# Kernel tuning notes

Hardware: AMD Instinct MI355X
Metric: run time of the kernel (lower is better)

## Reference

```python
import jax, jax.numpy as jnp
import numpy as np

B, N, C, D, H, O = 32, 2048, 16, 128, 128, 128


def setup_inputs():
    key = jax.random.key(0)
    ks = jax.random.split(key, 6)
    childrenList = jax.random.randint(ks[0], (B, N, C), 0, N)
    nodeEmb = jax.random.normal(ks[1], (B, N, D), dtype=jnp.float32)
    std1 = 1.0 / np.sqrt(D)
    W1 = jax.random.normal(ks[2], (3 * D, H), dtype=jnp.float32) * std1
    b1 = jax.random.normal(ks[3], (H,), dtype=jnp.float32) * (2.0 * std1)
    std2 = 1.0 / np.sqrt(H)
    W2 = jax.random.normal(ks[4], (H, O), dtype=jnp.float32) * std2
    b2 = jax.random.normal(ks[5], (O,), dtype=jnp.float32) * (2.0 * std2)
    return {"childrenList": childrenList, "nodeEmb": nodeEmb,
            "W1": W1, "b1": b1, "W2": W2, "b2": b2}


def _gather_feature(children, emb):
    # children: [B,N,C] int (0 = padding/no child), emb: [B,N,D]
    Bx, Nx, Dx = emb.shape
    # index 0 must look up a zero vector (padding child)
    lookup = jnp.concatenate([jnp.zeros((Bx, 1, Dx), emb.dtype), emb[:, 1:, :]], axis=1)
    child_emb = jax.vmap(lambda lu, ch: lu[ch])(lookup, children)      # [B,N,C,D]
    return jnp.concatenate([emb[:, :, None, :], child_emb], axis=2)    # [B,N,C+1,D]


def _conv_weights(children):
    # TBCNN positional coefficients eta_t / eta_r / eta_l (Mou et al.)
    Bx, Nx, Cx = children.shape
    f32 = jnp.float32
    mask = (children > 0).astype(f32)                                   # [B,N,C]
    t = jnp.concatenate([jnp.ones((Bx, Nx, 1), f32),
                         jnp.zeros((Bx, Nx, Cx), f32)], axis=2)        # parent=1, children=0
    num_sib = jnp.sum(mask, axis=2, keepdims=True)                      # [B,N,1]
    pos = jnp.arange(1, Cx + 1, dtype=f32)                              # 1-based child position
    r_child = jnp.where(num_sib == 1, 0.5 * mask,
                        mask * (pos - 1.0) / jnp.maximum(num_sib - 1.0, 1.0))
    r = jnp.concatenate([jnp.zeros((Bx, Nx, 1), f32), r_child], axis=2)
    full_mask = jnp.concatenate([jnp.ones((Bx, Nx, 1), f32), mask], axis=2)
    l = (1.0 - t) * (1.0 - r) * full_mask
    return jnp.stack([t, r, l], axis=-1)                                # [B,N,C+1,3]


def reference(childrenList, nodeEmb, W1, b1, W2, b2):
    feature = _gather_feature(childrenList, nodeEmb)                    # [B,N,C+1,D]
    weights = _conv_weights(childrenList)                               # [B,N,C+1,3]
    wf = jnp.einsum('bnck,bncd->bnkd', weights, feature)                # [B,N,3,D]
    wf = wf.reshape(wf.shape[0], wf.shape[1], -1)                       # [B,N,3D]
    h = jnp.tanh(wf @ W1 + b1)                                          # [B,N,H]
    pooled = jnp.max(h, axis=1)                                         # [B,H] max-pool over nodes
    out = jnp.tanh(pooled @ W2 + b2)                                    # [B,O]
    half = out.shape[0] // 2
    v1, v2 = out[:half], out[half:]
    eps = 1e-8
    n1 = jnp.maximum(jnp.linalg.norm(v1, axis=1), eps)
    n2 = jnp.maximum(jnp.linalg.norm(v2, axis=1), eps)
    return jnp.sum(v1 * v2, axis=1) / (n1 * n2)                         # [B/2]
```

## Files before the change

### kernel.cpp

```cpp
#include <hip/hip_runtime.h>

#define NB 32
#define NN 2048
#define NC 16
#define ND 128
#define NH 128
#define NK 384
#define TM 32
#define NBLK (NB * (NN / TM))

typedef __bf16 bf16x8 __attribute__((ext_vector_type(8)));
typedef float f32x4 __attribute__((ext_vector_type(4)));

__device__ __forceinline__ unsigned short f2bf(float f){
  unsigned u = __float_as_uint(f);
  u = (u + 0x7fffu + ((u >> 16) & 1u)) >> 16;
  return (unsigned short)u;
}
__device__ __forceinline__ unsigned enc_f32(float x){
  unsigned u = __float_as_uint(x);
  return (u & 0x80000000u) ? ~u : (u | 0x80000000u);
}
__device__ __forceinline__ float dec_f32(unsigned u){
  return __uint_as_float((u & 0x80000000u) ? (u & 0x7fffffffu) : ~u);
}

__device__ __forceinline__ void stq(unsigned char* base, int stride, int row, int koff, uint4 u){
  *(uint4*)(base + row * stride + (koff ^ ((row & 7) << 4))) = u;
}
__device__ __forceinline__ void st8(unsigned char* base, int stride, int row, int koff, const float* f){
  uint4 u;
  u.x = (unsigned)f2bf(f[0]) | ((unsigned)f2bf(f[1]) << 16);
  u.y = (unsigned)f2bf(f[2]) | ((unsigned)f2bf(f[3]) << 16);
  u.z = (unsigned)f2bf(f[4]) | ((unsigned)f2bf(f[5]) << 16);
  u.w = (unsigned)f2bf(f[6]) | ((unsigned)f2bf(f[7]) << 16);
  stq(base, stride, row, koff, u);
}
__device__ __forceinline__ uint4 ldq(const unsigned char* base, int stride, int row, int koff){
  return *(const uint4*)(base + row * stride + (koff ^ ((row & 7) << 4)));
}

#define OFF_POOLED 0
#define OFF_W1     16384
#define OFF_W2     114688
#define OFF_EMB    147456
#define WS_NEED_BF (147456 + (size_t)NB*NN*ND*2)

__global__ __launch_bounds__(256) void tbcnn_prep(
    const float* __restrict__ nodeEmb, const float* __restrict__ W1,
    const float* __restrict__ W2, unsigned* __restrict__ pooled,
    uint4* __restrict__ w1frag, uint4* __restrict__ w2frag,
    ushort* __restrict__ embBf, int doEmb)
{
  const int blk = blockIdx.x;
  const int t = threadIdx.x;
  if (blk < 2048){
    if (!doEmb) return;
    const float4* src = (const float4*)nodeEmb;
    const int tid = blk * 256 + t;
    #pragma unroll
    for (int it = 0; it < 4; ++it){
      const int i = tid + it * 524288;
      float4 v = src[i];
      ushort4 o;
      o.x = f2bf(v.x); o.y = f2bf(v.y); o.z = f2bf(v.z); o.w = f2bf(v.w);
      *(ushort4*)(embBf + (size_t)i * 4) = o;
    }
  } else if (blk < 2072){
    const int tt = (blk - 2048) * 256 + t;
    if (tt < NB * NH) pooled[tt] = 0u;
    const int lane = tt & 63;
    const int rest = tt >> 6;
    const int ks = rest % 12;
    const int cf = rest / 12;
    const int col = (cf >> 1) * 32 + (cf & 1) * 16 + (lane & 15);
    const int k0 = ks * 32 + (lane >> 4) * 8;
    unsigned ps[4];
    #pragma unroll
    for (int p = 0; p < 4; ++p){
      unsigned lo = f2bf(W1[(size_t)(k0 + 2*p) * NH + col]);
      unsigned hi = f2bf(W1[(size_t)(k0 + 2*p + 1) * NH + col]);
      ps[p] = lo | (hi << 16);
    }
    w1frag[tt] = make_uint4(ps[0], ps[1], ps[2], ps[3]);
  } else {
    const int tt = (blk - 2072) * 256 + t;
    const int lane = tt & 63;
    const int rest = tt >> 6;
    const int ks = rest & 3;
    const int cf = rest >> 2;
    const int col = (cf >> 1) * 32 + (cf & 1) * 16 + (lane & 15);
    const int k0 = ks * 32 + (lane >> 4) * 8;
    unsigned ps[4];
    #pragma unroll
    for (int p = 0; p < 4; ++p){
      unsigned lo = f2bf(W2[(size_t)(k0 + 2*p) * NH + col]);
      unsigned hi = f2bf(W2[(size_t)(k0 + 2*p + 1) * NH + col]);
      ps[p] = lo | (hi << 16);
    }
    w2frag[tt] = make_uint4(ps[0], ps[1], ps[2], ps[3]);
  }
}

#define PROCU(u, i) { \
  float lo_ = __uint_as_float((u) << 16); \
  float hi_ = __uint_as_float((u) & 0xffff0000u); \
  aR[(i)]   += wrc * lo_; aL[(i)]   += wlc * lo_; \
  aR[(i)+1] += wrc * hi_; aL[(i)+1] += wlc * hi_; }

template<bool BF>
__global__ __launch_bounds__(256, 2) void tbcnn_main(
    const int* __restrict__ children, const float* __restrict__ nodeEmb,
    const ushort* __restrict__ embBf, const uint4* __restrict__ w1frag,
    unsigned* __restrict__ pooled)
{
  __shared__ __align__(16) unsigned char wf_raw[TM * 768];
  const int j0 = ((blockIdx.x & 7) << 8) | (blockIdx.x >> 3);
  const int b    = j0 >> 6;
  const int tile = j0 & 63;
  const int n0 = tile * TM;
  const int t = threadIdx.x;
  const int lane = t & 63;
  const int w = t >> 6;

  {
    const int nloc = t >> 3;
    const int q = t & 7;
    const int d0 = q * 16;
    const int gn = n0 + nloc;
    const int4* chp4 = (const int4*)(children + ((size_t)b * NN + gn) * NC);

    int ns = 0;
    #pragma unroll
    for (int c4 = 0; c4 < 4; ++c4){
      int4 v = chp4[c4];
      ns += (v.x > 0) + (v.y > 0) + (v.z > 0) + (v.w > 0);
    }
    const float rdiv = 1.0f / (float)(((ns - 1) > 1) ? (ns - 1) : 1);
    const bool one_sib = (ns == 1);

    if (BF){
      const ushort* sp = embBf + ((size_t)b * NN + gn) * ND + d0;
      stq(wf_raw, 768, nloc, 2 * d0,       *(const uint4*)sp);
      stq(wf_raw, 768, nloc, 2 * (d0 + 8), *(const uint4*)(sp + 8));
    } else {
      const float* sp = nodeEmb + ((size_t)b * NN + gn) * ND + d0;
      float sv[16];
      #pragma unroll
      for (int j = 0; j < 4; ++j){
        float4 s = *(const float4*)(sp + j * 4);
        sv[j*4+0]=s.x; sv[j*4+1]=s.y; sv[j*4+2]=s.z; sv[j*4+3]=s.w;
      }
      st8(wf_raw, 768, nloc, 2 * d0, sv);
      st8(wf_raw, 768, nloc, 2 * (d0 + 8), sv + 8);
    }

    float aR[16], aL[16];
    #pragma unroll
    for (int i = 0; i < 16; ++i){ aR[i] = 0.0f; aL[i] = 0.0f; }
    #pragma unroll
    for (int c4 = 0; c4 < 4; ++c4){
      int4 v = chp4[c4];
      int cidx[4] = {v.x, v.y, v.z, v.w};
      #pragma unroll
      for (int jj = 0; jj < 4; ++jj){
        const int c = c4 * 4 + jj;
        const int idx = cidx[jj];
        const float mk  = (idx > 0) ? 1.0f : 0.0f;
        const float wrc = one_sib ? (0.5f * mk) : (mk * (float)c * rdiv);
        const float wlc = (1.0f - wrc) * mk;
        if (BF){
          const ushort* cp = embBf + ((size_t)b * NN + idx) * ND + d0;
          uint4 u0 = *(const uint4*)cp;
          uint4 u1 = *(const uint4*)(cp + 8);
          PROCU(u0.x, 0)  PROCU(u0.y, 2)  PROCU(u0.z, 4)  PROCU(u0.w, 6)
          PROCU(u1.x, 8)  PROCU(u1.y, 10) PROCU(u1.z, 12) PROCU(u1.w, 14)
        } else {
          const float* cp = nodeEmb + ((size_t)b * NN + idx) * ND + d0;
          #pragma unroll
          for (int j = 0; j < 4; ++j){
            float4 u = *(const float4*)(cp + j * 4);
            aR[j*4+0] += wrc * u.x; aL[j*4+0] += wlc * u.x;
            aR[j*4+1] += wrc * u.y; aL[j*4+1] += wlc * u.y;
            aR[j*4+2] += wrc * u.z; aL[j*4+2] += wlc * u.z;
            aR[j*4+3] += wrc * u.w; aL[j*4+3] += wlc * u.w;
          }
        }
      }
    }
    st8(wf_raw, 768, nloc, 2 * (ND + d0),         aR);
    st8(wf_raw, 768, nloc, 2 * (ND + d0 + 8),     aR + 8);
    st8(wf_raw, 768, nloc, 2 * (2 * ND + d0),     aL);
    st8(wf_raw, 768, nloc, 2 * (2 * ND + d0 + 8), aL + 8);
  }
  __syncthreads();

  f32x4 acc[2][2];
  #pragma unroll
  for (int rf = 0; rf < 2; ++rf){
    acc[rf][0] = (f32x4){0.f, 0.f, 0.f, 0.f};
    acc[rf][1] = (f32x4){0.f, 0.f, 0.f, 0.f};
  }
  #pragma unroll 4
  for (int ks = 0; ks < 12; ++ks){
    bf16x8 B0 = __builtin_bit_cast(bf16x8, w1frag[((w * 2 + 0) * 12 + ks) * 64 + lane]);
    bf16x8 B1 = __builtin_bit_cast(bf16x8, w1frag[((w * 2 + 1) * 12 + ks) * 64 + lane]);
    const int koff = ks * 64 + ((lane >> 4) << 4);
    #pragma unroll
    for (int rf = 0; rf < 2; ++rf){
      const int row = rf * 16 + (lane & 15);
      bf16x8 a = __builtin_bit_cast(bf16x8, ldq(wf_raw, 768, row, koff));
      acc[rf][0] = __builtin_amdgcn_mfma_f32_16x16x32_bf16(a, B0, acc[rf][0], 0, 0, 0);
      acc[rf][1] = __builtin_amdgcn_mfma_f32_16x16x32_bf16(a, B1, acc[rf][1], 0, 0, 0);
    }
  }

  float m0 = -3.0e38f, m1 = -3.0e38f;
  #pragma unroll
  for (int rf = 0; rf < 2; ++rf)
    #pragma unroll
    for (int i = 0; i < 4; ++i){
      m0 = fmaxf(m0, acc[rf][0][i]);
      m1 = fmaxf(m1, acc[rf][1][i]);
    }
  m0 = fmaxf(m0, __shfl_xor(m0, 16, 64));
  m0 = fmaxf(m0, __shfl_xor(m0, 32, 64));
  m1 = fmaxf(m1, __shfl_xor(m1, 16, 64));
  m1 = fmaxf(m1, __shfl_xor(m1, 32, 64));
  if (lane < 16){
    atomicMax(pooled + b * NH + w * 32 + lane,      enc_f32(m0));
    atomicMax(pooled + b * NH + w * 32 + 16 + lane, enc_f32(m1));
  }
}

__global__ __launch_bounds__(256) void tbcnn_final(
    const unsigned* __restrict__ pooled, const float* __restrict__ b1,
    const uint4* __restrict__ w2frag, const float* __restrict__ b2,
    float* __restrict__ out)
{
  __shared__ __align__(16) unsigned char hls[NB * 256];
  __shared__ float os[NB * NH];
  const int t = threadIdx.x;
  const int lane = t & 63;
  const int w = t >> 6;

  {
    const int row = t >> 3;
    const int q = t & 7;
    const int d0 = q * 16;
    const unsigned* pp = pooled + row * NH + d0;
    const float* bp = b1 + d0;
    float hv[16];
    #pragma unroll
    for (int j = 0; j < 16; ++j) hv[j] = tanhf(dec_f32(pp[j]) + bp[j]);
    st8(hls, 256, row, 2 * d0, hv);
    st8(hls, 256, row, 2 * (d0 + 8), hv + 8);
  }
  __syncthreads();

  f32x4 acc[2][2];
  #pragma unroll
  for (int rf = 0; rf < 2; ++rf){
    acc[rf][0] = (f32x4){0.f, 0.f, 0.f, 0.f};
    acc[rf][1] = (f32x4){0.f, 0.f, 0.f, 0.f};
  }
  #pragma unroll
  for (int ks = 0; ks < 4; ++ks){
    bf16x8 B0 = __builtin_bit_cast(bf16x8, w2frag[((w * 2 + 0) * 4 + ks) * 64 + lane]);
    bf16x8 B1 = __builtin_bit_cast(bf16x8, w2frag[((w * 2 + 1) * 4 + ks) * 64 + lane]);
    const int koff = ks * 64 + ((lane >> 4) << 4);
    #pragma unroll
    for (int rf = 0; rf < 2; ++rf){
      const int row = rf * 16 + (lane & 15);
      bf16x8 a = __builtin_bit_cast(bf16x8, ldq(hls, 256, row, koff));
      acc[rf][0] = __builtin_amdgcn_mfma_f32_16x16x32_bf16(a, B0, acc[rf][0], 0, 0, 0);
      acc[rf][1] = __builtin_amdgcn_mfma_f32_16x16x32_bf16(a, B1, acc[rf][1], 0, 0, 0);
    }
  }

  #pragma unroll
  for (int rf = 0; rf < 2; ++rf)
    #pragma unroll
    for (int cf = 0; cf < 2; ++cf){
      const int col = w * 32 + cf * 16 + (lane & 15);
      const float bias = b2[col];
      #pragma unroll
      for (int i = 0; i < 4; ++i){
        const int r = rf * 16 + (lane >> 4) * 4 + i;
        os[r * NH + col] = tanhf(acc[rf][cf][i] + bias);
      }
    }
  __syncthreads();

  if (t < 16){
    float s12 = 0.f, s11 = 0.f, s22 = 0.f;
    #pragma unroll 4
    for (int d = 0; d < NH; ++d){
      float a = os[t * NH + d];
      float c = os[(t + 16) * NH + d];
      s12 += a * c; s11 += a * a; s22 += c * c;
    }
    float n1 = fmaxf(sqrtf(s11), 1e-8f);
    float n2 = fmaxf(sqrtf(s22), 1e-8f);
    out[t] = s12 / (n1 * n2);
  }
}

extern "C" void kernel_launch(void* const* d_in, const int* in_sizes, int n_in,
                              void* d_out, int out_size, void* d_ws, size_t ws_size,
                              hipStream_t stream)
{
  const int*   children = (const int*)d_in[0];
  const float* nodeEmb  = (const float*)d_in[1];
  const float* W1       = (const float*)d_in[2];
  const float* b1       = (const float*)d_in[3];
  const float* W2       = (const float*)d_in[4];
  const float* b2       = (const float*)d_in[5];
  float* out = (float*)d_out;

  unsigned* pooled = (unsigned*)((char*)d_ws + OFF_POOLED);
  uint4* w1frag    = (uint4*)((char*)d_ws + OFF_W1);
  uint4* w2frag    = (uint4*)((char*)d_ws + OFF_W2);
  ushort* embBf    = (ushort*)((char*)d_ws + OFF_EMB);

  const bool bf = (ws_size >= WS_NEED_BF);

  tbcnn_prep<<<2080, 256, 0, stream>>>(nodeEmb, W1, W2, pooled, w1frag, w2frag, embBf, bf ? 1 : 0);
  if (bf)
    tbcnn_main<true><<<NBLK, 256, 0, stream>>>(children, nodeEmb, embBf, w1frag, pooled);
  else
    tbcnn_main<false><<<NBLK, 256, 0, stream>>>(children, nodeEmb, embBf, w1frag, pooled);
  tbcnn_final<<<1, 256, 0, stream>>>(pooled, b1, w2frag, b2, out);
}
```

Before: 49.45 us.

## Fuse final MLP into main kernel via last-block counter, widen blocks to 512 threads

Removes the separate final kernel launch: each main block increments a global done counter and the last block computes the W2 layer, tanh and cosine similarity, reading pooled values via atomics. The main kernel now uses 512 threads per 32-node tile, so each thread gathers 8 features instead of 16 and each wave computes one 16-column MFMA slice. The prep kernel's embedding conversion is remapped so the chunks it writes follow the main kernel's block order. The cost is an extra atomic and two barriers per block, plus a serial tail in the last block; the wider blocks trade register pressure for more threads sharing each tile.

```diff
diff --git a/kernel.cpp b/kernel.cpp
--- a/kernel.cpp
+++ b/kernel.cpp
@@ -43,24 +43,25 @@
 #define OFF_POOLED 0
 #define OFF_W1     16384
 #define OFF_W2     114688
-#define OFF_EMB    147456
-#define WS_NEED_BF (147456 + (size_t)NB*NN*ND*2)
+#define OFF_DONE   147456
+#define OFF_EMB    147712
+#define WS_NEED_BF (OFF_EMB + (size_t)NB*NN*ND*2)
 
 __global__ __launch_bounds__(256) void tbcnn_prep(
     const float* __restrict__ nodeEmb, const float* __restrict__ W1,
     const float* __restrict__ W2, unsigned* __restrict__ pooled,
     uint4* __restrict__ w1frag, uint4* __restrict__ w2frag,
-    ushort* __restrict__ embBf, int doEmb)
+    ushort* __restrict__ embBf, unsigned* __restrict__ done, int doEmb)
 {
   const int blk = blockIdx.x;
   const int t = threadIdx.x;
   if (blk < 2048){
     if (!doEmb) return;
+    const int chk = ((blk & 7) << 8) | (blk >> 3);
     const float4* src = (const float4*)nodeEmb;
-    const int tid = blk * 256 + t;
     #pragma unroll
     for (int it = 0; it < 4; ++it){
-      const int i = tid + it * 524288;
+      const int i = chk * 1024 + it * 256 + t;
       float4 v = src[i];
       ushort4 o;
       o.x = f2bf(v.x); o.y = f2bf(v.y); o.z = f2bf(v.z); o.w = f2bf(v.w);
@@ -69,6 +70,7 @@
   } else if (blk < 2072){
     const int tt = (blk - 2048) * 256 + t;
     if (tt < NB * NH) pooled[tt] = 0u;
+    if (tt == NB * NH) *done = 0u;
     const int lane = tt & 63;
     const int rest = tt >> 6;
     const int ks = rest % 12;
@@ -109,24 +111,26 @@
   aR[(i)+1] += wrc * hi_; aL[(i)+1] += wlc * hi_; }
 
 template<bool BF>
-__global__ __launch_bounds__(256, 2) void tbcnn_main(
+__global__ __launch_bounds__(512, 8) void tbcnn_main(
     const int* __restrict__ children, const float* __restrict__ nodeEmb,
     const ushort* __restrict__ embBf, const uint4* __restrict__ w1frag,
-    unsigned* __restrict__ pooled)
+    const uint4* __restrict__ w2frag, const float* __restrict__ b1,
+    const float* __restrict__ b2, unsigned* __restrict__ pooled,
+    unsigned* __restrict__ done, float* __restrict__ out)
 {
   __shared__ __align__(16) unsigned char wf_raw[TM * 768];
+  __shared__ unsigned last_flag;
   const int j0 = ((blockIdx.x & 7) << 8) | (blockIdx.x >> 3);
   const int b    = j0 >> 6;
-  const int tile = j0 & 63;
-  const int n0 = tile * TM;
+  const int n0 = (j0 & 63) * TM;
   const int t = threadIdx.x;
   const int lane = t & 63;
   const int w = t >> 6;
 
   {
-    const int nloc = t >> 3;
-    const int q = t & 7;
-    const int d0 = q * 16;
+    const int nloc = t >> 4;
+    const int q = t & 15;
+    const int d0 = q * 8;
     const int gn = n0 + nloc;
     const int4* chp4 = (const int4*)(children + ((size_t)b * NN + gn) * NC);
 
@@ -138,26 +142,24 @@
     }
     const float rdiv = 1.0f / (float)(((ns - 1) > 1) ? (ns - 1) : 1);
     const bool one_sib = (ns == 1);
+    const size_t rowbase = (size_t)b * NN;
 
     if (BF){
-      const ushort* sp = embBf + ((size_t)b * NN + gn) * ND + d0;
-      stq(wf_raw, 768, nloc, 2 * d0,       *(const uint4*)sp);
-      stq(wf_raw, 768, nloc, 2 * (d0 + 8), *(const uint4*)(sp + 8));
+      const ushort* sp = embBf + (rowbase + gn) * ND + d0;
+      stq(wf_raw, 768, nloc, 2 * d0, *(const uint4*)sp);
     } else {
-      const float* sp = nodeEmb + ((size_t)b * NN + gn) * ND + d0;
-      float sv[16];
-      #pragma unroll
-      for (int j = 0; j < 4; ++j){
-        float4 s = *(const float4*)(sp + j * 4);
-        sv[j*4+0]=s.x; sv[j*4+1]=s.y; sv[j*4+2]=s.z; sv[j*4+3]=s.w;
-      }
+      const float* sp = nodeEmb + (rowbase + gn) * ND + d0;
+      float sv[8];
+      float4 s0 = *(const float4*)sp;
+      float4 s1 = *(const float4*)(sp + 4);
+      sv[0]=s0.x; sv[1]=s0.y; sv[2]=s0.z; sv[3]=s0.w;
+      sv[4]=s1.x; sv[5]=s1.y; sv[6]=s1.z; sv[7]=s1.w;
       st8(wf_raw, 768, nloc, 2 * d0, sv);
-      st8(wf_raw, 768, nloc, 2 * (d0 + 8), sv + 8);
-    }
-
-    float aR[16], aL[16];
-    #pragma unroll
-    for (int i = 0; i < 16; ++i){ aR[i] = 0.0f; aL[i] = 0.0f; }
+    }
+
+    float aR[8], aL[8];
+    #pragma unroll
+    for (int i = 0; i < 8; ++i){ aR[i] = 0.0f; aL[i] = 0.0f; }
     #pragma unroll
     for (int c4 = 0; c4 < 4; ++c4){
       int4 v = chp4[c4];
@@ -170,128 +172,110 @@
         const float wrc = one_sib ? (0.5f * mk) : (mk * (float)c * rdiv);
         const float wlc = (1.0f - wrc) * mk;
         if (BF){
-          const ushort* cp = embBf + ((size_t)b * NN + idx) * ND + d0;
-          uint4 u0 = *(const uint4*)cp;
-          uint4 u1 = *(const uint4*)(cp + 8);
-          PROCU(u0.x, 0)  PROCU(u0.y, 2)  PROCU(u0.z, 4)  PROCU(u0.w, 6)
-          PROCU(u1.x, 8)  PROCU(u1.y, 10) PROCU(u1.z, 12) PROCU(u1.w, 14)
+          uint4 u = *(const uint4*)(embBf + (rowbase + idx) * ND + d0);
+          PROCU(u.x, 0) PROCU(u.y, 2) PROCU(u.z, 4) PROCU(u.w, 6)
         } else {
-          const float* cp = nodeEmb + ((size_t)b * NN + idx) * ND + d0;
-          #pragma unroll
-          for (int j = 0; j < 4; ++j){
-            float4 u = *(const float4*)(cp + j * 4);
-            aR[j*4+0] += wrc * u.x; aL[j*4+0] += wlc * u.x;
-            aR[j*4+1] += wrc * u.y; aL[j*4+1] += wlc * u.y;
-            aR[j*4+2] += wrc * u.z; aL[j*4+2] += wlc * u.z;
-            aR[j*4+3] += wrc * u.w; aL[j*4+3] += wlc * u.w;
-          }
+          const float* cp = nodeEmb + (rowbase + idx) * ND + d0;
+          float4 u0 = *(const float4*)cp;
+          float4 u1 = *(const float4*)(cp + 4);
+          aR[0] += wrc * u0.x; aL[0] += wlc * u0.x;
+          aR[1] += wrc * u0.y; aL[1] += wlc * u0.y;
+          aR[2] += wrc * u0.z; aL[2] += wlc * u0.z;
+          aR[3] += wrc * u0.w; aL[3] += wlc * u0.w;
+          aR[4] += wrc * u1.x; aL[4] += wlc * u1.x;
+          aR[5] += wrc * u1.y; aL[5] += wlc * u1.y;
+          aR[6] += wrc * u1.z; aL[6] += wlc * u1.z;
+          aR[7] += wrc * u1.w; aL[7] += wlc * u1.w;
         }
       }
     }
-    st8(wf_raw, 768, nloc, 2 * (ND + d0),         aR);
-    st8(wf_raw, 768, nloc, 2 * (ND + d0 + 8),     aR + 8);
-    st8(wf_raw, 768, nloc, 2 * (2 * ND + d0),     aL);
-    st8(wf_raw, 768, nloc, 2 * (2 * ND + d0 + 8), aL + 8);
-  }
-  __syncthreads();
-
-  f32x4 acc[2][2];
-  #pragma unroll
-  for (int rf = 0; rf < 2; ++rf){
-    acc[rf][0] = (f32x4){0.f, 0.f, 0.f, 0.f};
-    acc[rf][1] = (f32x4){0.f, 0.f, 0.f, 0.f};
-  }
-  #pragma unroll 4
-  for (int ks = 0; ks < 12; ++ks){
-    bf16x8 B0 = __builtin_bit_cast(bf16x8, w1frag[((w * 2 + 0) * 12 + ks) * 64 + lane]);
-    bf16x8 B1 = __builtin_bit_cast(bf16x8, w1frag[((w * 2 + 1) * 12 + ks) * 64 + lane]);
-    const int koff = ks * 64 + ((lane >> 4) << 4);
-    #pragma unroll
-    for (int rf = 0; rf < 2; ++rf){
-      const int row = rf * 16 + (lane & 15);
-      bf16x8 a = __builtin_bit_cast(bf16x8, ldq(wf_raw, 768, row, koff));
-      acc[rf][0] = __builtin_amdgcn_mfma_f32_16x16x32_bf16(a, B0, acc[rf][0], 0, 0, 0);
-      acc[rf][1] = __builtin_amdgcn_mfma_f32_16x16x32_bf16(a, B1, acc[rf][1], 0, 0, 0);
-    }
-  }
-
-  float m0 = -3.0e38f, m1 = -3.0e38f;
-  #pragma unroll
-  for (int rf = 0; rf < 2; ++rf)
+    st8(wf_raw, 768, nloc, 2 * (ND + d0),     aR);
+    st8(wf_raw, 768, nloc, 2 * (2 * ND + d0), aL);
+  }
+  __syncthreads();
+
+  {
+    f32x4 acc0 = (f32x4){0.f,0.f,0.f,0.f};
+    f32x4 acc1 = (f32x4){0.f,0.f,0.f,0.f};
+    #pragma unroll 4
+    for (int ks = 0; ks < 12; ++ks){
+      bf16x8 B0 = __builtin_bit_cast(bf16x8, w1frag[(w * 12 + ks) * 64 + lane]);
+      const int koff = ks * 64 + ((lane >> 4) << 4);
+      bf16x8 a0 = __builtin_bit_cast(bf16x8, ldq(wf_raw, 768, (lane & 15),      koff));
+      bf16x8 a1 = __builtin_bit_cast(bf16x8, ldq(wf_raw, 768, 16 + (lane & 15), koff));
+      acc0 = __builtin_amdgcn_mfma_f32_16x16x32_bf16(a0, B0, acc0, 0, 0, 0);
+      acc1 = __builtin_amdgcn_mfma_f32_16x16x32_bf16(a1, B0, acc1, 0, 0, 0);
+    }
+    float m = -3.0e38f;
     #pragma unroll
     for (int i = 0; i < 4; ++i){
-      m0 = fmaxf(m0, acc[rf][0][i]);
-      m1 = fmaxf(m1, acc[rf][1][i]);
-    }
-  m0 = fmaxf(m0, __shfl_xor(m0, 16, 64));
-  m0 = fmaxf(m0, __shfl_xor(m0, 32, 64));
-  m1 = fmaxf(m1, __shfl_xor(m1, 16, 64));
-  m1 = fmaxf(m1, __shfl_xor(m1, 32, 64));
-  if (lane < 16){
-    atomicMax(pooled + b * NH + w * 32 + lane,      enc_f32(m0));
-    atomicMax(pooled + b * NH + w * 32 + 16 + lane, enc_f32(m1));
-  }
-}
-
-__global__ __launch_bounds__(256) void tbcnn_final(
-    const unsigned* __restrict__ pooled, const float* __restrict__ b1,
-    const uint4* __restrict__ w2frag, const float* __restrict__ b2,
-    float* __restrict__ out)
-{
-  __shared__ __align__(16) unsigned char hls[NB * 256];
-  __shared__ float os[NB * NH];
-  const int t = threadIdx.x;
-  const int lane = t & 63;
-  const int w = t >> 6;
-
-  {
+      m = fmaxf(m, acc0[i]);
+      m = fmaxf(m, acc1[i]);
+    }
+    m = fmaxf(m, __shfl_xor(m, 16, 64));
+    m = fmaxf(m, __shfl_xor(m, 32, 64));
+    const int colbase = (w >> 1) * 32 + (w & 1) * 16;
+    if (lane < 16)
+      atomicMax(pooled + b * NH + colbase + lane, enc_f32(m));
+  }
+
+  __syncthreads();
+  if (t == 0){
+    __threadfence();
+    unsigned r = atomicAdd(done, 1u);
+    last_flag = (r == NBLK - 1) ? 1u : 0u;
+  }
+  __syncthreads();
+  if (!last_flag) return;
+
+  unsigned char* hls = wf_raw;
+  float* os = (float*)(wf_raw + 8192);
+  if (t < 256){
     const int row = t >> 3;
     const int q = t & 7;
     const int d0 = q * 16;
-    const unsigned* pp = pooled + row * NH + d0;
+    unsigned* pp = pooled + row * NH + d0;
     const float* bp = b1 + d0;
     float hv[16];
     #pragma unroll
-    for (int j = 0; j < 16; ++j) hv[j] = tanhf(dec_f32(pp[j]) + bp[j]);
+    for (int j = 0; j < 16; ++j) hv[j] = tanhf(dec_f32(atomicMax(pp + j, 0u)) + bp[j]);
     st8(hls, 256, row, 2 * d0, hv);
     st8(hls, 256, row, 2 * (d0 + 8), hv + 8);
   }
   __syncthreads();
-
-  f32x4 acc[2][2];
-  #pragma unroll
-  for (int rf = 0; rf < 2; ++rf){
-    acc[rf][0] = (f32x4){0.f, 0.f, 0.f, 0.f};
-    acc[rf][1] = (f32x4){0.f, 0.f, 0.f, 0.f};
-  }
-  #pragma unroll
-  for (int ks = 0; ks < 4; ++ks){
-    bf16x8 B0 = __builtin_bit_cast(bf16x8, w2frag[((w * 2 + 0) * 4 + ks) * 64 + lane]);
-    bf16x8 B1 = __builtin_bit_cast(bf16x8, w2frag[((w * 2 + 1) * 4 + ks) * 64 + lane]);
-    const int koff = ks * 64 + ((lane >> 4) << 4);
+  if (t < 256){
+    f32x4 acc[2][2];
     #pragma unroll
     for (int rf = 0; rf < 2; ++rf){
-      const int row = rf * 16 + (lane & 15);
-      bf16x8 a = __builtin_bit_cast(bf16x8, ldq(hls, 256, row, koff));
-      acc[rf][0] = __builtin_amdgcn_mfma_f32_16x16x32_bf16(a, B0, acc[rf][0], 0, 0, 0);
-      acc[rf][1] = __builtin_amdgcn_mfma_f32_16x16x32_bf16(a, B1, acc[rf][1], 0, 0, 0);
-    }
-  }
-
-  #pragma unroll
-  for (int rf = 0; rf < 2; ++rf)
-    #pragma unroll
-    for (int cf = 0; cf < 2; ++cf){
-      const int col = w * 32 + cf * 16 + (lane & 15);
-      const float bias = b2[col];
+      acc[rf][0] = (f32x4){0.f,0.f,0.f,0.f};
+      acc[rf][1] = (f32x4){0.f,0.f,0.f,0.f};
+    }
+    #pragma unroll
+    for (int ks = 0; ks < 4; ++ks){
+      bf16x8 B0 = __builtin_bit_cast(bf16x8, w2frag[((w * 2 + 0) * 4 + ks) * 64 + lane]);
+      bf16x8 B1 = __builtin_bit_cast(bf16x8, w2frag[((w * 2 + 1) * 4 + ks) * 64 + lane]);
+      const int koff = ks * 64 + ((lane >> 4) << 4);
       #pragma unroll
-      for (int i = 0; i < 4; ++i){
-        const int r = rf * 16 + (lane >> 4) * 4 + i;
-        os[r * NH + col] = tanhf(acc[rf][cf][i] + bias);
+      for (int rf = 0; rf < 2; ++rf){
+        bf16x8 a = __builtin_bit_cast(bf16x8, ldq(hls, 256, rf * 16 + (lane & 15), koff));
+        acc[rf][0] = __builtin_amdgcn_mfma_f32_16x16x32_bf16(a, B0, acc[rf][0], 0, 0, 0);
+        acc[rf][1] = __builtin_amdgcn_mfma_f32_16x16x32_bf16(a, B1, acc[rf][1], 0, 0, 0);
       }
     }
-  __syncthreads();
-
+    #pragma unroll
+    for (int rf = 0; rf < 2; ++rf)
+      #pragma unroll
+      for (int cf = 0; cf < 2; ++cf){
+        const int col = w * 32 + cf * 16 + (lane & 15);
+        const float bias = b2[col];
+        #pragma unroll
+        for (int i = 0; i < 4; ++i){
+          const int r = rf * 16 + (lane >> 4) * 4 + i;
+          os[r * NH + col] = tanhf(acc[rf][cf][i] + bias);
+        }
+      }
+  }
+  __syncthreads();
   if (t < 16){
     float s12 = 0.f, s11 = 0.f, s22 = 0.f;
     #pragma unroll 4
@@ -321,14 +305,14 @@
   unsigned* pooled = (unsigned*)((char*)d_ws + OFF_POOLED);
   uint4* w1frag    = (uint4*)((char*)d_ws + OFF_W1);
   uint4* w2frag    = (uint4*)((char*)d_ws + OFF_W2);
+  unsigned* done   = (unsigned*)((char*)d_ws + OFF_DONE);
   ushort* embBf    = (ushort*)((char*)d_ws + OFF_EMB);
 
   const bool bf = (ws_size >= WS_NEED_BF);
 
-  tbcnn_prep<<<2080, 256, 0, stream>>>(nodeEmb, W1, W2, pooled, w1frag, w2frag, embBf, bf ? 1 : 0);
+  tbcnn_prep<<<2080, 256, 0, stream>>>(nodeEmb, W1, W2, pooled, w1frag, w2frag, embBf, done, bf ? 1 : 0);
   if (bf)
-    tbcnn_main<true><<<NBLK, 256, 0, stream>>>(children, nodeEmb, embBf, w1frag, pooled);
+    tbcnn_main<true><<<NBLK, 512, 0, stream>>>(children, nodeEmb, embBf, w1frag, w2frag, b1, b2, pooled, done, out);
   else
-    tbcnn_main<false><<<NBLK, 256, 0, stream>>>(children, nodeEmb, embBf, w1frag, pooled);
-  tbcnn_final<<<1, 256, 0, stream>>>(pooled, b1, w2frag, b2, out);
-}
+    tbcnn_main<false><<<NBLK, 512, 0, stream>>>(children, nodeEmb, embBf, w1frag, w2frag, b1, b2, pooled, done, out);
+}
```

Measured after the change: 193.8 us. 292% more time.

## Fuse final projection into main kernel via last-block completion counter

Applied to the files above, without the earlier changes.

Removes the separate single-block final kernel: each main block increments a global done counter after its atomicMax pooling, and the last block to finish computes tanh, the W2 MFMA, and the cosine similarity, reusing the shared-memory tile. The counter is reset in the prep kernel. The prep kernel's emb conversion is also reordered so blocks convert contiguous chunks in the same interleaved order as main's blocks. This trades one launch for an extra atomic per block and a serialized tail in one block.

```diff
diff --git a/kernel.cpp b/kernel.cpp
--- a/kernel.cpp
+++ b/kernel.cpp
@@ -43,24 +43,25 @@
 #define OFF_POOLED 0
 #define OFF_W1     16384
 #define OFF_W2     114688
-#define OFF_EMB    147456
-#define WS_NEED_BF (147456 + (size_t)NB*NN*ND*2)
+#define OFF_DONE   147456
+#define OFF_EMB    147712
+#define WS_NEED_BF (OFF_EMB + (size_t)NB*NN*ND*2)
 
 __global__ __launch_bounds__(256) void tbcnn_prep(
     const float* __restrict__ nodeEmb, const float* __restrict__ W1,
     const float* __restrict__ W2, unsigned* __restrict__ pooled,
     uint4* __restrict__ w1frag, uint4* __restrict__ w2frag,
-    ushort* __restrict__ embBf, int doEmb)
+    ushort* __restrict__ embBf, unsigned* __restrict__ done, int doEmb)
 {
   const int blk = blockIdx.x;
   const int t = threadIdx.x;
   if (blk < 2048){
     if (!doEmb) return;
+    const int chk = ((blk & 7) << 8) | (blk >> 3);
     const float4* src = (const float4*)nodeEmb;
-    const int tid = blk * 256 + t;
     #pragma unroll
     for (int it = 0; it < 4; ++it){
-      const int i = tid + it * 524288;
+      const int i = chk * 1024 + it * 256 + t;
       float4 v = src[i];
       ushort4 o;
       o.x = f2bf(v.x); o.y = f2bf(v.y); o.z = f2bf(v.z); o.w = f2bf(v.w);
@@ -69,6 +70,7 @@
   } else if (blk < 2072){
     const int tt = (blk - 2048) * 256 + t;
     if (tt < NB * NH) pooled[tt] = 0u;
+    if (tt == NB * NH) *done = 0u;
     const int lane = tt & 63;
     const int rest = tt >> 6;
     const int ks = rest % 12;
@@ -112,13 +114,15 @@
 __global__ __launch_bounds__(256, 2) void tbcnn_main(
     const int* __restrict__ children, const float* __restrict__ nodeEmb,
     const ushort* __restrict__ embBf, const uint4* __restrict__ w1frag,
-    unsigned* __restrict__ pooled)
+    const uint4* __restrict__ w2frag, const float* __restrict__ b1,
+    const float* __restrict__ b2, unsigned* __restrict__ pooled,
+    unsigned* __restrict__ done, float* __restrict__ out)
 {
   __shared__ __align__(16) unsigned char wf_raw[TM * 768];
+  __shared__ unsigned last_flag;
   const int j0 = ((blockIdx.x & 7) << 8) | (blockIdx.x >> 3);
   const int b    = j0 >> 6;
-  const int tile = j0 & 63;
-  const int n0 = tile * TM;
+  const int n0 = (j0 & 63) * TM;
   const int t = threadIdx.x;
   const int lane = t & 63;
   const int w = t >> 6;
@@ -138,13 +142,14 @@
     }
     const float rdiv = 1.0f / (float)(((ns - 1) > 1) ? (ns - 1) : 1);
     const bool one_sib = (ns == 1);
+    const size_t rowbase = (size_t)b * NN;
 
     if (BF){
-      const ushort* sp = embBf + ((size_t)b * NN + gn) * ND + d0;
+      const ushort* sp = embBf + (rowbase + gn) * ND + d0;
       stq(wf_raw, 768, nloc, 2 * d0,       *(const uint4*)sp);
       stq(wf_raw, 768, nloc, 2 * (d0 + 8), *(const uint4*)(sp + 8));
     } else {
-      const float* sp = nodeEmb + ((size_t)b * NN + gn) * ND + d0;
+      const float* sp = nodeEmb + (rowbase + gn) * ND + d0;
       float sv[16];
       #pragma unroll
       for (int j = 0; j < 4; ++j){
@@ -170,13 +175,13 @@
         const float wrc = one_sib ? (0.5f * mk) : (mk * (float)c * rdiv);
         const float wlc = (1.0f - wrc) * mk;
         if (BF){
-          const ushort* cp = embBf + ((size_t)b * NN + idx) * ND + d0;
+          const ushort* cp = embBf + (rowbase + idx) * ND + d0;
           uint4 u0 = *(const uint4*)cp;
           uint4 u1 = *(const uint4*)(cp + 8);
           PROCU(u0.x, 0)  PROCU(u0.y, 2)  PROCU(u0.z, 4)  PROCU(u0.w, 6)
           PROCU(u1.x, 8)  PROCU(u1.y, 10) PROCU(u1.z, 12) PROCU(u1.w, 14)
         } else {
-          const float* cp = nodeEmb + ((size_t)b * NN + idx) * ND + d0;
+          const float* cp = nodeEmb + (rowbase + idx) * ND + d0;
           #pragma unroll
           for (int j = 0; j < 4; ++j){
             float4 u = *(const float4*)(cp + j * 4);
@@ -195,103 +200,101 @@
   }
   __syncthreads();
 
-  f32x4 acc[2][2];
-  #pragma unroll
-  for (int rf = 0; rf < 2; ++rf){
-    acc[rf][0] = (f32x4){0.f, 0.f, 0.f, 0.f};
-    acc[rf][1] = (f32x4){0.f, 0.f, 0.f, 0.f};
-  }
-  #pragma unroll 4
-  for (int ks = 0; ks < 12; ++ks){
-    bf16x8 B0 = __builtin_bit_cast(bf16x8, w1frag[((w * 2 + 0) * 12 + ks) * 64 + lane]);
-    bf16x8 B1 = __builtin_bit_cast(bf16x8, w1frag[((w * 2 + 1) * 12 + ks) * 64 + lane]);
-    const int koff = ks * 64 + ((lane >> 4) << 4);
+  {
+    f32x4 acc[2][2];
     #pragma unroll
     for (int rf = 0; rf < 2; ++rf){
-      const int row = rf * 16 + (lane & 15);
-      bf16x8 a = __builtin_bit_cast(bf16x8, ldq(wf_raw, 768, row, koff));
-      acc[rf][0] = __builtin_amdgcn_mfma_f32_16x16x32_bf16(a, B0, acc[rf][0], 0, 0, 0);
-      acc[rf][1] = __builtin_amdgcn_mfma_f32_16x16x32_bf16(a, B1, acc[rf][1], 0, 0, 0);
-    }
-  }
-
-  float m0 = -3.0e38f, m1 = -3.0e38f;
-  #pragma unroll
-  for (int rf = 0; rf < 2; ++rf)
-    #pragma unroll
-    for (int i = 0; i < 4; ++i){
-      m0 = fmaxf(m0, acc[rf][0][i]);
-      m1 = fmaxf(m1, acc[rf][1][i]);
-    }
-  m0 = fmaxf(m0, __shfl_xor(m0, 16, 64));
-  m0 = fmaxf(m0, __shfl_xor(m0, 32, 64));
-  m1 = fmaxf(m1, __shfl_xor(m1, 16, 64));
-  m1 = fmaxf(m1, __shfl_xor(m1, 32, 64));
-  if (lane < 16){
-    atomicMax(pooled + b * NH + w * 32 + lane,      enc_f32(m0));
-    atomicMax(pooled + b * NH + w * 32 + 16 + lane, enc_f32(m1));
-  }
-}
-
-__global__ __launch_bounds__(256) void tbcnn_final(
-    const unsigned* __restrict__ pooled, const float* __restrict__ b1,
-    const uint4* __restrict__ w2frag, const float* __restrict__ b2,
-    float* __restrict__ out)
-{
-  __shared__ __align__(16) unsigned char hls[NB * 256];
-  __shared__ float os[NB * NH];
-  const int t = threadIdx.x;
-  const int lane = t & 63;
-  const int w = t >> 6;
-
+      acc[rf][0] = (f32x4){0.f, 0.f, 0.f, 0.f};
+      acc[rf][1] = (f32x4){0.f, 0.f, 0.f, 0.f};
+    }
+    #pragma unroll 4
+    for (int ks = 0; ks < 12; ++ks){
+      bf16x8 B0 = __builtin_bit_cast(bf16x8, w1frag[((w * 2 + 0) * 12 + ks) * 64 + lane]);
+      bf16x8 B1 = __builtin_bit_cast(bf16x8, w1frag[((w * 2 + 1) * 12 + ks) * 64 + lane]);
+      const int koff = ks * 64 + ((lane >> 4) << 4);
+      #pragma unroll
+      for (int rf = 0; rf < 2; ++rf){
+        const int row = rf * 16 + (lane & 15);
+        bf16x8 a = __builtin_bit_cast(bf16x8, ldq(wf_raw, 768, row, koff));
+        acc[rf][0] = __builtin_amdgcn_mfma_f32_16x16x32_bf16(a, B0, acc[rf][0], 0, 0, 0);
+        acc[rf][1] = __builtin_amdgcn_mfma_f32_16x16x32_bf16(a, B1, acc[rf][1], 0, 0, 0);
+      }
+    }
+
+    float m0 = -3.0e38f, m1 = -3.0e38f;
+    #pragma unroll
+    for (int rf = 0; rf < 2; ++rf)
+      #pragma unroll
+      for (int i = 0; i < 4; ++i){
+        m0 = fmaxf(m0, acc[rf][0][i]);
+        m1 = fmaxf(m1, acc[rf][1][i]);
+      }
+    m0 = fmaxf(m0, __shfl_xor(m0, 16, 64));
+    m0 = fmaxf(m0, __shfl_xor(m0, 32, 64));
+    m1 = fmaxf(m1, __shfl_xor(m1, 16, 64));
+    m1 = fmaxf(m1, __shfl_xor(m1, 32, 64));
+    if (lane < 16){
+      atomicMax(pooled + b * NH + w * 32 + lane,      enc_f32(m0));
+      atomicMax(pooled + b * NH + w * 32 + 16 + lane, enc_f32(m1));
+    }
+  }
+
+  __syncthreads();
+  if (t == 0){
+    unsigned r = atomicAdd(done, 1u);
+    last_flag = (r == NBLK - 1) ? 1u : 0u;
+  }
+  __syncthreads();
+  if (!last_flag) return;
+
+  unsigned char* hls = wf_raw;
+  float* os = (float*)(wf_raw + 8192);
   {
     const int row = t >> 3;
     const int q = t & 7;
     const int d0 = q * 16;
-    const unsigned* pp = pooled + row * NH + d0;
+    unsigned* pp = pooled + row * NH + d0;
     const float* bp = b1 + d0;
     float hv[16];
     #pragma unroll
-    for (int j = 0; j < 16; ++j) hv[j] = tanhf(dec_f32(pp[j]) + bp[j]);
+    for (int j = 0; j < 16; ++j) hv[j] = tanhf(dec_f32(atomicMax(pp + j, 0u)) + bp[j]);
     st8(hls, 256, row, 2 * d0, hv);
     st8(hls, 256, row, 2 * (d0 + 8), hv + 8);
   }
   __syncthreads();
-
-  f32x4 acc[2][2];
-  #pragma unroll
-  for (int rf = 0; rf < 2; ++rf){
-    acc[rf][0] = (f32x4){0.f, 0.f, 0.f, 0.f};
-    acc[rf][1] = (f32x4){0.f, 0.f, 0.f, 0.f};
-  }
-  #pragma unroll
-  for (int ks = 0; ks < 4; ++ks){
-    bf16x8 B0 = __builtin_bit_cast(bf16x8, w2frag[((w * 2 + 0) * 4 + ks) * 64 + lane]);
-    bf16x8 B1 = __builtin_bit_cast(bf16x8, w2frag[((w * 2 + 1) * 4 + ks) * 64 + lane]);
-    const int koff = ks * 64 + ((lane >> 4) << 4);
+  {
+    f32x4 acc[2][2];
     #pragma unroll
     for (int rf = 0; rf < 2; ++rf){
-      const int row = rf * 16 + (lane & 15);
-      bf16x8 a = __builtin_bit_cast(bf16x8, ldq(hls, 256, row, koff));
-      acc[rf][0] = __builtin_amdgcn_mfma_f32_16x16x32_bf16(a, B0, acc[rf][0], 0, 0, 0);
-      acc[rf][1] = __builtin_amdgcn_mfma_f32_16x16x32_bf16(a, B1, acc[rf][1], 0, 0, 0);
-    }
-  }
-
-  #pragma unroll
-  for (int rf = 0; rf < 2; ++rf)
-    #pragma unroll
-    for (int cf = 0; cf < 2; ++cf){
-      const int col = w * 32 + cf * 16 + (lane & 15);
-      const float bias = b2[col];
-      #pragma unroll
-      for (int i = 0; i < 4; ++i){
-        const int r = rf * 16 + (lane >> 4) * 4 + i;
-        os[r * NH + col] = tanhf(acc[rf][cf][i] + bias);
-      }
-    }
-  __syncthreads();
-
+      acc[rf][0] = (f32x4){0.f,0.f,0.f,0.f};
+      acc[rf][1] = (f32x4){0.f,0.f,0.f,0.f};
+    }
+    #pragma unroll
+    for (int ks = 0; ks < 4; ++ks){
+      bf16x8 B0 = __builtin_bit_cast(bf16x8, w2frag[((w * 2 + 0) * 4 + ks) * 64 + lane]);
+      bf16x8 B1 = __builtin_bit_cast(bf16x8, w2frag[((w * 2 + 1) * 4 + ks) * 64 + lane]);
+      const int koff = ks * 64 + ((lane >> 4) << 4);
+      #pragma unroll
+      for (int rf = 0; rf < 2; ++rf){
+        bf16x8 a = __builtin_bit_cast(bf16x8, ldq(hls, 256, rf * 16 + (lane & 15), koff));
+        acc[rf][0] = __builtin_amdgcn_mfma_f32_16x16x32_bf16(a, B0, acc[rf][0], 0, 0, 0);
+        acc[rf][1] = __builtin_amdgcn_mfma_f32_16x16x32_bf16(a, B1, acc[rf][1], 0, 0, 0);
+      }
+    }
+    #pragma unroll
+    for (int rf = 0; rf < 2; ++rf)
+      #pragma unroll
+      for (int cf = 0; cf < 2; ++cf){
+        const int col = w * 32 + cf * 16 + (lane & 15);
+        const float bias = b2[col];
+        #pragma unroll
+        for (int i = 0; i < 4; ++i){
+          const int r = rf * 16 + (lane >> 4) * 4 + i;
+          os[r * NH + col] = tanhf(acc[rf][cf][i] + bias);
+        }
+      }
+  }
+  __syncthreads();
   if (t < 16){
     float s12 = 0.f, s11 = 0.f, s22 = 0.f;
     #pragma unroll 4
@@ -321,14 +324,14 @@
   unsigned* pooled = (unsigned*)((char*)d_ws + OFF_POOLED);
   uint4* w1frag    = (uint4*)((char*)d_ws + OFF_W1);
   uint4* w2frag    = (uint4*)((char*)d_ws + OFF_W2);
+  unsigned* done   = (unsigned*)((char*)d_ws + OFF_DONE);
   ushort* embBf    = (ushort*)((char*)d_ws + OFF_EMB);
 
   const bool bf = (ws_size >= WS_NEED_BF);
 
-  tbcnn_prep<<<2080, 256, 0, stream>>>(nodeEmb, W1, W2, pooled, w1frag, w2frag, embBf, bf ? 1 : 0);
+  tbcnn_prep<<<2080, 256, 0, stream>>>(nodeEmb, W1, W2, pooled, w1frag, w2frag, embBf, done, bf ? 1 : 0);
   if (bf)
-    tbcnn_main<true><<<NBLK, 256, 0, stream>>>(children, nodeEmb, embBf, w1frag, pooled);
+    tbcnn_main<true><<<NBLK, 256, 0, stream>>>(children, nodeEmb, embBf, w1frag, w2frag, b1, b2, pooled, done, out);
   else
-    tbcnn_main<false><<<NBLK, 256, 0, stream>>>(children, nodeEmb, embBf, w1frag, pooled);
-  tbcnn_final<<<1, 256, 0, stream>>>(pooled, b1, w2frag, b2, out);
-}
+    tbcnn_main<false><<<NBLK, 256, 0, stream>>>(children, nodeEmb, embBf, w1frag, w2frag, b1, b2, pooled, done, out);
+}
```

Result: slower. 57.11 us (+15.5%).

## Restructure bf16 child gather so each wave handles whole rows with coalesced loads

Applied to the files above, without the earlier changes.

In the bf16 path of the main kernel, each wave now processes 8 node rows in turn. Every lane loads one 32-bit chunk (two bf16 values) of the parent and of all 16 child rows, so each child row is read as one 256-byte coalesced access per wave instead of 16-byte pieces scattered across threads. A scheduling barrier issues all 17 loads before any math, and the accumulation uses packed float2 operations. The prep kernel's conversion loop is also remapped so each block converts a contiguous chunk, with block indices swizzled the same way as the main kernel. The trade-off is more, smaller load instructions and more registers held per lane.

```diff
diff --git a/kernel.cpp b/kernel.cpp
--- a/kernel.cpp
+++ b/kernel.cpp
@@ -5,12 +5,12 @@
 #define NC 16
 #define ND 128
 #define NH 128
-#define NK 384
 #define TM 32
 #define NBLK (NB * (NN / TM))
 
 typedef __bf16 bf16x8 __attribute__((ext_vector_type(8)));
 typedef float f32x4 __attribute__((ext_vector_type(4)));
+typedef float f32x2 __attribute__((ext_vector_type(2)));
 
 __device__ __forceinline__ unsigned short f2bf(float f){
   unsigned u = __float_as_uint(f);
@@ -44,7 +44,7 @@
 #define OFF_W1     16384
 #define OFF_W2     114688
 #define OFF_EMB    147456
-#define WS_NEED_BF (147456 + (size_t)NB*NN*ND*2)
+#define WS_NEED_BF (OFF_EMB + (size_t)NB*NN*ND*2)
 
 __global__ __launch_bounds__(256) void tbcnn_prep(
     const float* __restrict__ nodeEmb, const float* __restrict__ W1,
@@ -56,11 +56,11 @@
   const int t = threadIdx.x;
   if (blk < 2048){
     if (!doEmb) return;
+    const int chk = ((blk & 7) << 8) | (blk >> 3);
     const float4* src = (const float4*)nodeEmb;
-    const int tid = blk * 256 + t;
     #pragma unroll
     for (int it = 0; it < 4; ++it){
-      const int i = tid + it * 524288;
+      const int i = chk * 1024 + it * 256 + t;
       float4 v = src[i];
       ushort4 o;
       o.x = f2bf(v.x); o.y = f2bf(v.y); o.z = f2bf(v.z); o.w = f2bf(v.w);
@@ -102,11 +102,17 @@
   }
 }
 
-#define PROCU(u, i) { \
-  float lo_ = __uint_as_float((u) << 16); \
-  float hi_ = __uint_as_float((u) & 0xffff0000u); \
-  aR[(i)]   += wrc * lo_; aL[(i)]   += wlc * lo_; \
-  aR[(i)+1] += wrc * hi_; aL[(i)+1] += wlc * hi_; }
+#define GLD(idx) (*(const unsigned*)(embBf + (rowbase + (unsigned)(idx)) * ND + (lane << 1)))
+
+#define PRC(k, idx, creg) { \
+  const float mk  = ((idx) > 0) ? 1.0f : 0.0f; \
+  const float wrc = one_sib ? (0.5f * mk) : (mk * (float)(k) * rdiv); \
+  const float wlc = (1.0f - wrc) * mk; \
+  f32x2 x_; \
+  x_[0] = __uint_as_float((creg) << 16); \
+  x_[1] = __uint_as_float((creg) & 0xffff0000u); \
+  aR += (f32x2){wrc, wrc} * x_; \
+  aL += (f32x2){wlc, wlc} * x_; }
 
 template<bool BF>
 __global__ __launch_bounds__(256, 2) void tbcnn_main(
@@ -116,20 +122,54 @@
 {
   __shared__ __align__(16) unsigned char wf_raw[TM * 768];
   const int j0 = ((blockIdx.x & 7) << 8) | (blockIdx.x >> 3);
-  const int b    = j0 >> 6;
-  const int tile = j0 & 63;
-  const int n0 = tile * TM;
+  const int b = j0 >> 6;
+  const int n0 = (j0 & 63) * TM;
   const int t = threadIdx.x;
   const int lane = t & 63;
   const int w = t >> 6;
-
-  {
+  const size_t rowbase = (size_t)b * NN;
+
+  if (BF){
+    #pragma unroll
+    for (int p = 0; p < 8; ++p){
+      const int row = (w << 3) + p;
+      const int gn = n0 + row;
+      const int4* chp4 = (const int4*)(children + (rowbase + gn) * NC);
+      const int4 v0 = chp4[0], v1 = chp4[1], v2 = chp4[2], v3 = chp4[3];
+      int ns = (v0.x>0)+(v0.y>0)+(v0.z>0)+(v0.w>0)
+             + (v1.x>0)+(v1.y>0)+(v1.z>0)+(v1.w>0)
+             + (v2.x>0)+(v2.y>0)+(v2.z>0)+(v2.w>0)
+             + (v3.x>0)+(v3.y>0)+(v3.z>0)+(v3.w>0);
+      const float rdiv = 1.0f / (float)(((ns - 1) > 1) ? (ns - 1) : 1);
+      const bool one_sib = (ns == 1);
+
+      const unsigned sv = GLD(gn);
+      const unsigned c0  = GLD(v0.x), c1  = GLD(v0.y), c2  = GLD(v0.z), c3  = GLD(v0.w);
+      const unsigned c4  = GLD(v1.x), c5  = GLD(v1.y), c6  = GLD(v1.z), c7  = GLD(v1.w);
+      const unsigned c8  = GLD(v2.x), c9  = GLD(v2.y), c10 = GLD(v2.z), c11 = GLD(v2.w);
+      const unsigned c12 = GLD(v3.x), c13 = GLD(v3.y), c14 = GLD(v3.z), c15 = GLD(v3.w);
+      __builtin_amdgcn_sched_barrier(0);
+
+      f32x2 aR = (f32x2){0.f,0.f}, aL = (f32x2){0.f,0.f};
+      PRC(0,  v0.x, c0)  PRC(1,  v0.y, c1)  PRC(2,  v0.z, c2)  PRC(3,  v0.w, c3)
+      PRC(4,  v1.x, c4)  PRC(5,  v1.y, c5)  PRC(6,  v1.z, c6)  PRC(7,  v1.w, c7)
+      PRC(8,  v2.x, c8)  PRC(9,  v2.y, c9)  PRC(10, v2.z, c10) PRC(11, v2.w, c11)
+      PRC(12, v3.x, c12) PRC(13, v3.y, c13) PRC(14, v3.z, c14) PRC(15, v3.w, c15)
+
+      const unsigned uR = (unsigned)f2bf(aR[0]) | ((unsigned)f2bf(aR[1]) << 16);
+      const unsigned uL = (unsigned)f2bf(aL[0]) | ((unsigned)f2bf(aL[1]) << 16);
+      const int sw = (row & 7) << 4;
+      unsigned char* rp = wf_raw + row * 768;
+      *(unsigned*)(rp + (((lane << 2)      ) ^ sw)) = sv;
+      *(unsigned*)(rp + ((256 + (lane << 2)) ^ sw)) = uR;
+      *(unsigned*)(rp + ((512 + (lane << 2)) ^ sw)) = uL;
+    }
+  } else {
     const int nloc = t >> 3;
     const int q = t & 7;
     const int d0 = q * 16;
     const int gn = n0 + nloc;
-    const int4* chp4 = (const int4*)(children + ((size_t)b * NN + gn) * NC);
-
+    const int4* chp4 = (const int4*)(children + (rowbase + gn) * NC);
     int ns = 0;
     #pragma unroll
     for (int c4 = 0; c4 < 4; ++c4){
@@ -138,23 +178,15 @@
     }
     const float rdiv = 1.0f / (float)(((ns - 1) > 1) ? (ns - 1) : 1);
     const bool one_sib = (ns == 1);
-
-    if (BF){
-      const ushort* sp = embBf + ((size_t)b * NN + gn) * ND + d0;
-      stq(wf_raw, 768, nloc, 2 * d0,       *(const uint4*)sp);
-      stq(wf_raw, 768, nloc, 2 * (d0 + 8), *(const uint4*)(sp + 8));
-    } else {
-      const float* sp = nodeEmb + ((size_t)b * NN + gn) * ND + d0;
-      float sv[16];
-      #pragma unroll
-      for (int j = 0; j < 4; ++j){
-        float4 s = *(const float4*)(sp + j * 4);
-        sv[j*4+0]=s.x; sv[j*4+1]=s.y; sv[j*4+2]=s.z; sv[j*4+3]=s.w;
-      }
-      st8(wf_raw, 768, nloc, 2 * d0, sv);
-      st8(wf_raw, 768, nloc, 2 * (d0 + 8), sv + 8);
-    }
-
+    const float* sp = nodeEmb + (rowbase + gn) * ND + d0;
+    float sv[16];
+    #pragma unroll
+    for (int j = 0; j < 4; ++j){
+      float4 s = *(const float4*)(sp + j * 4);
+      sv[j*4+0]=s.x; sv[j*4+1]=s.y; sv[j*4+2]=s.z; sv[j*4+3]=s.w;
+    }
+    st8(wf_raw, 768, nloc, 2 * d0, sv);
+    st8(wf_raw, 768, nloc, 2 * (d0 + 8), sv + 8);
     float aR[16], aL[16];
     #pragma unroll
     for (int i = 0; i < 16; ++i){ aR[i] = 0.0f; aL[i] = 0.0f; }
@@ -169,22 +201,14 @@
         const float mk  = (idx > 0) ? 1.0f : 0.0f;
         const float wrc = one_sib ? (0.5f * mk) : (mk * (float)c * rdiv);
         const float wlc = (1.0f - wrc) * mk;
-        if (BF){
-          const ushort* cp = embBf + ((size_t)b * NN + idx) * ND + d0;
-          uint4 u0 = *(const uint4*)cp;
-          uint4 u1 = *(const uint4*)(cp + 8);
-          PROCU(u0.x, 0)  PROCU(u0.y, 2)  PROCU(u0.z, 4)  PROCU(u0.w, 6)
-          PROCU(u1.x, 8)  PROCU(u1.y, 10) PROCU(u1.z, 12) PROCU(u1.w, 14)
-        } else {
-          const float* cp = nodeEmb + ((size_t)b * NN + idx) * ND + d0;
-          #pragma unroll
-          for (int j = 0; j < 4; ++j){
-            float4 u = *(const float4*)(cp + j * 4);
-            aR[j*4+0] += wrc * u.x; aL[j*4+0] += wlc * u.x;
-            aR[j*4+1] += wrc * u.y; aL[j*4+1] += wlc * u.y;
-            aR[j*4+2] += wrc * u.z; aL[j*4+2] += wlc * u.z;
-            aR[j*4+3] += wrc * u.w; aL[j*4+3] += wlc * u.w;
-          }
+        const float* cp = nodeEmb + (rowbase + idx) * ND + d0;
+        #pragma unroll
+        for (int j = 0; j < 4; ++j){
+          float4 u = *(const float4*)(cp + j * 4);
+          aR[j*4+0] += wrc * u.x; aL[j*4+0] += wlc * u.x;
+          aR[j*4+1] += wrc * u.y; aL[j*4+1] += wlc * u.y;
+          aR[j*4+2] += wrc * u.z; aL[j*4+2] += wlc * u.z;
+          aR[j*4+3] += wrc * u.w; aL[j*4+3] += wlc * u.w;
         }
       }
     }
@@ -195,41 +219,43 @@
   }
   __syncthreads();
 
-  f32x4 acc[2][2];
-  #pragma unroll
-  for (int rf = 0; rf < 2; ++rf){
-    acc[rf][0] = (f32x4){0.f, 0.f, 0.f, 0.f};
-    acc[rf][1] = (f32x4){0.f, 0.f, 0.f, 0.f};
-  }
-  #pragma unroll 4
-  for (int ks = 0; ks < 12; ++ks){
-    bf16x8 B0 = __builtin_bit_cast(bf16x8, w1frag[((w * 2 + 0) * 12 + ks) * 64 + lane]);
-    bf16x8 B1 = __builtin_bit_cast(bf16x8, w1frag[((w * 2 + 1) * 12 + ks) * 64 + lane]);
-    const int koff = ks * 64 + ((lane >> 4) << 4);
+  {
+    f32x4 acc[2][2];
     #pragma unroll
     for (int rf = 0; rf < 2; ++rf){
-      const int row = rf * 16 + (lane & 15);
-      bf16x8 a = __builtin_bit_cast(bf16x8, ldq(wf_raw, 768, row, koff));
-      acc[rf][0] = __builtin_amdgcn_mfma_f32_16x16x32_bf16(a, B0, acc[rf][0], 0, 0, 0);
-      acc[rf][1] = __builtin_amdgcn_mfma_f32_16x16x32_bf16(a, B1, acc[rf][1], 0, 0, 0);
-    }
-  }
-
-  float m0 = -3.0e38f, m1 = -3.0e38f;
-  #pragma unroll
-  for (int rf = 0; rf < 2; ++rf)
-    #pragma unroll
-    for (int i = 0; i < 4; ++i){
-      m0 = fmaxf(m0, acc[rf][0][i]);
-      m1 = fmaxf(m1, acc[rf][1][i]);
-    }
-  m0 = fmaxf(m0, __shfl_xor(m0, 16, 64));
-  m0 = fmaxf(m0, __shfl_xor(m0, 32, 64));
-  m1 = fmaxf(m1, __shfl_xor(m1, 16, 64));
-  m1 = fmaxf(m1, __shfl_xor(m1, 32, 64));
-  if (lane < 16){
-    atomicMax(pooled + b * NH + w * 32 + lane,      enc_f32(m0));
-    atomicMax(pooled + b * NH + w * 32 + 16 + lane, enc_f32(m1));
+      acc[rf][0] = (f32x4){0.f, 0.f, 0.f, 0.f};
+      acc[rf][1] = (f32x4){0.f, 0.f, 0.f, 0.f};
+    }
+    #pragma unroll 4
+    for (int ks = 0; ks < 12; ++ks){
+      bf16x8 B0 = __builtin_bit_cast(bf16x8, w1frag[((w * 2 + 0) * 12 + ks) * 64 + lane]);
+      bf16x8 B1 = __builtin_bit_cast(bf16x8, w1frag[((w * 2 + 1) * 12 + ks) * 64 + lane]);
+      const int koff = ks * 64 + ((lane >> 4) << 4);
+      #pragma unroll
+      for (int rf = 0; rf < 2; ++rf){
+        const int row = rf * 16 + (lane & 15);
+        bf16x8 a = __builtin_bit_cast(bf16x8, ldq(wf_raw, 768, row, koff));
+        acc[rf][0] = __builtin_amdgcn_mfma_f32_16x16x32_bf16(a, B0, acc[rf][0], 0, 0, 0);
+        acc[rf][1] = __builtin_amdgcn_mfma_f32_16x16x32_bf16(a, B1, acc[rf][1], 0, 0, 0);
+      }
+    }
+
+    float m0 = -3.0e38f, m1 = -3.0e38f;
+    #pragma unroll
+    for (int rf = 0; rf < 2; ++rf)
+      #pragma unroll
+      for (int i = 0; i < 4; ++i){
+        m0 = fmaxf(m0, acc[rf][0][i]);
+        m1 = fmaxf(m1, acc[rf][1][i]);
+      }
+    m0 = fmaxf(m0, __shfl_xor(m0, 16, 64));
+    m0 = fmaxf(m0, __shfl_xor(m0, 32, 64));
+    m1 = fmaxf(m1, __shfl_xor(m1, 16, 64));
+    m1 = fmaxf(m1, __shfl_xor(m1, 32, 64));
+    if (lane < 16){
+      atomicMax(pooled + b * NH + w * 32 + lane,      enc_f32(m0));
+      atomicMax(pooled + b * NH + w * 32 + 16 + lane, enc_f32(m1));
+    }
   }
 }
 
@@ -257,41 +283,39 @@
     st8(hls, 256, row, 2 * (d0 + 8), hv + 8);
   }
   __syncthreads();
-
-  f32x4 acc[2][2];
-  #pragma unroll
-  for (int rf = 0; rf < 2; ++rf){
-    acc[rf][0] = (f32x4){0.f, 0.f, 0.f, 0.f};
-    acc[rf][1] = (f32x4){0.f, 0.f, 0.f, 0.f};
-  }
-  #pragma unroll
-  for (int ks = 0; ks < 4; ++ks){
-    bf16x8 B0 = __builtin_bit_cast(bf16x8, w2frag[((w * 2 + 0) * 4 + ks) * 64 + lane]);
-    bf16x8 B1 = __builtin_bit_cast(bf16x8, w2frag[((w * 2 + 1) * 4 + ks) * 64 + lane]);
-    const int koff = ks * 64 + ((lane >> 4) << 4);
+  {
+    f32x4 acc[2][2];
     #pragma unroll
     for (int rf = 0; rf < 2; ++rf){
-      const int row = rf * 16 + (lane & 15);
-      bf16x8 a = __builtin_bit_cast(bf16x8, ldq(hls, 256, row, koff));
-      acc[rf][0] = __builtin_amdgcn_mfma_f32_16x16x32_bf16(a, B0, acc[rf][0], 0, 0, 0);
-      acc[rf][1] = __builtin_amdgcn_mfma_f32_16x16x32_bf16(a, B1, acc[rf][1], 0, 0, 0);
-    }
-  }
-
-  #pragma unroll
-  for (int rf = 0; rf < 2; ++rf)
-    #pragma unroll
-    for (int cf = 0; cf < 2; ++cf){
-      const int col = w * 32 + cf * 16 + (lane & 15);
-      const float bias = b2[col];
-      #pragma unroll
-      for (int i = 0; i < 4; ++i){
-        const int r = rf * 16 + (lane >> 4) * 4 + i;
-        os[r * NH + col] = tanhf(acc[rf][cf][i] + bias);
-      }
-    }
+      acc[rf][0] = (f32x4){0.f,0.f,0.f,0.f};
+      acc[rf][1] = (f32x4){0.f,0.f,0.f,0.f};
+    }
+    #pragma unroll
+    for (int ks = 0; ks < 4; ++ks){
+      bf16x8 B0 = __builtin_bit_cast(bf16x8, w2frag[((w * 2 + 0) * 4 + ks) * 64 + lane]);
+      bf16x8 B1 = __builtin_bit_cast(bf16x8, w2frag[((w * 2 + 1) * 4 + ks) * 64 + lane]);
+      const int koff = ks * 64 + ((lane >> 4) << 4);
+      #pragma unroll
+      for (int rf = 0; rf < 2; ++rf){
+        bf16x8 a = __builtin_bit_cast(bf16x8, ldq(hls, 256, rf * 16 + (lane & 15), koff));
+        acc[rf][0] = __builtin_amdgcn_mfma_f32_16x16x32_bf16(a, B0, acc[rf][0], 0, 0, 0);
+        acc[rf][1] = __builtin_amdgcn_mfma_f32_16x16x32_bf16(a, B1, acc[rf][1], 0, 0, 0);
+      }
+    }
+    #pragma unroll
+    for (int rf = 0; rf < 2; ++rf)
+      #pragma unroll
+      for (int cf = 0; cf < 2; ++cf){
+        const int col = w * 32 + cf * 16 + (lane & 15);
+        const float bias = b2[col];
+        #pragma unroll
+        for (int i = 0; i < 4; ++i){
+          const int r = rf * 16 + (lane >> 4) * 4 + i;
+          os[r * NH + col] = tanhf(acc[rf][cf][i] + bias);
+        }
+      }
+  }
   __syncthreads();
-
   if (t < 16){
     float s12 = 0.f, s11 = 0.f, s22 = 0.f;
     #pragma unroll 4
```

Result: slower. 60.35 us (+22.0%).
